# Optimization experiments

Hardware: AMD Instinct MI355X
Metric: run time of the kernel (lower is better)

Reference implementation:

```python
import jax, jax.numpy as jnp
import numpy as np

B, N, M, G = 2, 8192, 8192, 256
X_MIN = Y_MIN = -35.0
CELL = abs(2.0 * X_MIN / G)  # cell size, as in construct_batched_cuda_grid


def setup_inputs() -> dict:
    key = jax.random.key(0)
    k1, k2, k3, k4, k5 = jax.random.split(key, 5)
    p_i = jax.random.uniform(k1, (B, N, 3), jnp.float32, -34.0, 34.0)
    p_j = jax.random.uniform(k2, (B, M, 3), jnp.float32, -34.0, 34.0)
    mos = jax.random.normal(k3, (B, 2, G, G), jnp.float32)
    error_p_i_flow = jax.random.uniform(k4, (B, N), jnp.float32)
    nearest_flow = jax.random.randint(k5, (B, N, 1), 0, M, jnp.int32)
    return {"p_i": p_i, "mos": mos, "p_j": p_j,
            "error_p_i_flow": error_p_i_flow, "nearest_flow": nearest_flow}


def _knn1_l1(x, y):
    # brute-force 1-NN with L1 (norm=1) distance, matching knn_points(..., K=1, norm=1)
    # build (B,N,M) dist one coordinate at a time to avoid a (B,N,M,3) intermediate
    d = (jnp.abs(x[:, :, None, 0] - y[:, None, :, 0])
         + jnp.abs(x[:, :, None, 1] - y[:, None, :, 1])
         + jnp.abs(x[:, :, None, 2] - y[:, None, :, 2]))
    return jnp.min(d, axis=-1), jnp.argmin(d, axis=-1)


def reference(p_i, mos, p_j, error_p_i_flow, nearest_flow):
    # NN_loss with reduction='none' -> error_p_i_rigid = (cham_x + cham_y)/2 (needs N==M)
    cham_x, nearest_rigid = _knn1_l1(p_i, p_j)  # (B,N), (B,N)
    cham_y, _ = _knn1_l1(p_j, p_i)              # (B,M)
    error_p_i_rigid = (cham_x + cham_y) * 0.5

    dynamic = error_p_i_flow > error_p_i_rigid             # (B,N) bool
    idx = jnp.where(dynamic, nearest_flow[..., 0], nearest_rigid)  # (B,N)
    art_labels = dynamic.astype(jnp.int32)                 # (B,N) in {0,1}

    # batched gather p_j[b, idx[b]]
    p_j_by_nn = jnp.take_along_axis(p_j, idx[..., None], axis=1)  # (B,N,3)

    # construct_batched_cuda_grid: scatter labels into (B,G,G), -1 elsewhere
    shift = jnp.array([X_MIN, Y_MIN], jnp.float32)
    cell_idx = ((p_j_by_nn[:, :, :2] - shift) / CELL).astype(jnp.int32)  # (B,N,2)
    bs = jnp.repeat(jnp.arange(B), N)
    grid = -jnp.ones((B, G, G), jnp.int32)
    grid = grid.at[bs,
                   cell_idx[..., 0].reshape(-1),
                   cell_idx[..., 1].reshape(-1)].set(art_labels.reshape(-1))

    # CrossEntropyLoss(ignore_index=-1), mean over non-ignored cells
    logp = jax.nn.log_softmax(mos, axis=1)                 # (B,C,G,G)
    valid = grid >= 0
    tgt = jnp.clip(grid, 0, None)
    lp = jnp.take_along_axis(logp, tgt[:, None], axis=1)[:, 0]  # (B,G,G)
    loss = -jnp.where(valid, lp, 0.0).sum() / jnp.maximum(valid.sum(), 1).astype(lp.dtype)
    return loss
```

## Files before the change

kernel.cpp:

```cpp
#include <hip/hip_runtime.h>
#include <float.h>

#define B_ 2
#define N_ 8192
#define G_ 256
constexpr float X_MIN_F = -35.0f;
constexpr float CELL_F  = 0.2734375f;

using u64 = unsigned long long;

#define OFF_CHAMY 131072
#define OFF_GRID  196608
#define OFF_ACCUM 720896

__global__ __launch_bounds__(256) void init_kernel(uint4* __restrict__ ws)
{
    int i = blockIdx.x * 256 + threadIdx.x;
    if (i < 45056)       ws[i] = make_uint4(~0u, ~0u, ~0u, ~0u);
    else if (i == 45056) ws[i] = make_uint4(0u, 0u, 0u, 0u);
}

template<bool NEED_IDX>
__global__ __launch_bounds__(256) void nn_kernel(const float* __restrict__ P,
                                                 const float* __restrict__ Q,
                                                 u64* __restrict__ outp,
                                                 unsigned* __restrict__ outd)
{
    const int b    = blockIdx.z;
    const int tid  = threadIdx.x;
    const int row0 = blockIdx.x * 1024 + tid * 4;
    const int c0   = blockIdx.y * 128;

    __shared__ __align__(16) float q[128 * 3];
    if (tid < 96)
        ((float4*)q)[tid] = ((const float4*)(Q + ((size_t)b * N_ + c0) * 3))[tid];

    const float4* pp = (const float4*)(P + ((size_t)b * N_ + row0) * 3);
    float4 r0 = pp[0], r1 = pp[1], r2 = pp[2];
    float px[4] = {r0.x, r0.w, r1.z, r2.y};
    float py[4] = {r0.y, r1.x, r1.w, r2.z};
    float pz[4] = {r0.z, r1.y, r2.x, r2.w};

    float best[4]; int bidx[4];
#pragma unroll
    for (int r = 0; r < 4; r++) { best[r] = FLT_MAX; bidx[r] = c0; }

    __syncthreads();

    for (int j4 = 0; j4 < 128; j4 += 4) {
        float4 a  = *(const float4*)&q[j4 * 3];
        float4 bb = *(const float4*)&q[j4 * 3 + 4];
        float4 cc = *(const float4*)&q[j4 * 3 + 8];
        float qxs[4] = {a.x, a.w, bb.z, cc.y};
        float qys[4] = {a.y, bb.x, bb.w, cc.z};
        float qzs[4] = {a.z, bb.y, cc.x, cc.w};
#pragma unroll
        for (int k = 0; k < 4; k++) {
#pragma unroll
            for (int r = 0; r < 4; r++) {
                float d = (fabsf(px[r] - qxs[k]) + fabsf(py[r] - qys[k]))
                          + fabsf(pz[r] - qzs[k]);
                if (NEED_IDX) {
                    bool lt = d < best[r];
                    best[r] = lt ? d : best[r];
                    bidx[r] = lt ? (c0 + j4 + k) : bidx[r];
                } else {
                    best[r] = fminf(best[r], d);
                }
            }
        }
    }

#pragma unroll
    for (int r = 0; r < 4; r++) {
        if (NEED_IDX) {
            u64 pk = ((u64)__float_as_uint(best[r]) << 32) | (unsigned)bidx[r];
            atomicMin(&outp[(size_t)b * N_ + row0 + r], pk);
        } else {
            atomicMin(&outd[(size_t)b * N_ + row0 + r], __float_as_uint(best[r]));
        }
    }
}

__global__ __launch_bounds__(256) void scatter_kernel(
    const u64* __restrict__ chamx, const unsigned* __restrict__ chamy,
    const float* __restrict__ flow, const int* __restrict__ nflow,
    const float* __restrict__ Pj, int* __restrict__ grid)
{
    int i = blockIdx.x * 256 + threadIdx.x;
    int b = i >> 13;
    int n = i & (N_ - 1);

    u64 pX = chamx[i];
    float dx = __uint_as_float((unsigned)(pX >> 32));
    float dy = __uint_as_float(chamy[i]);
    float rigid = (dx + dy) * 0.5f;

    bool dyn  = flow[i] > rigid;
    int label = dyn ? 1 : 0;
    int idx   = dyn ? nflow[i] : (int)(unsigned)(pX & 0xFFFFFFFFull);

    const float* qp = Pj + ((size_t)b * N_ + idx) * 3;
    float x = qp[0], y = qp[1];

    int cx = (int)((x - X_MIN_F) / CELL_F);
    int cy = (int)((y - X_MIN_F) / CELL_F);

    atomicMax(&grid[(b << 16) + cx * G_ + cy], (n << 1) | label);
}

__global__ __launch_bounds__(256) void ce_kernel(const float* __restrict__ mos,
                                                 const int* __restrict__ grid,
                                                 float* __restrict__ accum,
                                                 float* __restrict__ out)
{
    int i = blockIdx.x * 256 + threadIdx.x;
    float lsum = 0.0f;
    int   lcnt = 0;

    int packed = grid[i];
    if (packed >= 0) {
        int b    = i >> 16;
        int cell = i & 0xFFFF;
        float m0 = mos[((size_t)b * 2 + 0) * 65536 + cell];
        float m1 = mos[((size_t)b * 2 + 1) * 65536 + cell];
        float mx = fmaxf(m0, m1);
        float lse = logf(expf(m0 - mx) + expf(m1 - mx));
        float sh  = ((packed & 1) ? m1 : m0) - mx;
        lsum = sh - lse;
        lcnt = 1;
    }

#pragma unroll
    for (int o = 32; o > 0; o >>= 1) {
        lsum += __shfl_down(lsum, o);
        lcnt += __shfl_down(lcnt, o);
    }
    __shared__ float wsum[4];
    __shared__ int   wcnt[4];
    int wave = threadIdx.x >> 6;
    if ((threadIdx.x & 63) == 0) { wsum[wave] = lsum; wcnt[wave] = lcnt; }
    __syncthreads();
    if (threadIdx.x == 0) {
        float s = wsum[0] + wsum[1] + wsum[2] + wsum[3];
        int   c = wcnt[0] + wcnt[1] + wcnt[2] + wcnt[3];
        atomicAdd(&accum[0], s);
        atomicAdd((int*)&accum[1], c);
        __threadfence();
        unsigned t = atomicAdd((unsigned*)&accum[2], 1u);
        if (t == gridDim.x - 1) {
            float S = atomicAdd(&accum[0], 0.0f);
            int   C = atomicAdd((int*)&accum[1], 0);
            out[0] = -S / (float)(C > 0 ? C : 1);
        }
    }
}

extern "C" void kernel_launch(void* const* d_in, const int* in_sizes, int n_in,
                              void* d_out, int out_size, void* d_ws, size_t ws_size,
                              hipStream_t stream)
{
    const float* p_i   = (const float*)d_in[0];
    const float* mos   = (const float*)d_in[1];
    const float* p_j   = (const float*)d_in[2];
    const float* flow  = (const float*)d_in[3];
    const int*   nflow = (const int*)d_in[4];
    float* out = (float*)d_out;

    char* ws = (char*)d_ws;
    u64*      chamx = (u64*)(ws);
    unsigned* chamy = (unsigned*)(ws + OFF_CHAMY);
    int*      grid  = (int*)(ws + OFF_GRID);
    float*    accum = (float*)(ws + OFF_ACCUM);

    init_kernel<<<177, 256, 0, stream>>>((uint4*)ws);

    dim3 g(N_ / 1024, N_ / 128, B_);
    nn_kernel<true ><<<g, 256, 0, stream>>>(p_i, p_j, chamx, nullptr);
    nn_kernel<false><<<g, 256, 0, stream>>>(p_j, p_i, nullptr, chamy);

    scatter_kernel<<<(B_ * N_) / 256, 256, 0, stream>>>(chamx, chamy, flow,
                                                        nflow, p_j, grid);
    ce_kernel<<<(B_ * G_ * G_) / 256, 256, 0, stream>>>(mos, grid, accum, out);
}
```

Baseline: 144.4 us.

## Merge both NN directions into one launch and replace atomics with partial-min buffers

Both nearest-neighbour directions now run in a single kernel launch, with the direction chosen by blockIdx.z. Instead of 64 column chunks doing atomicMin per row, each block handles a larger column chunk (CC of 32 or 4, picked from workspace size) and writes its partial min to its own slot. The scatter kernel then reduces these partials before labelling. This removes one launch and the contention on global atomics, and init now only clears the grid. In exchange it uses more workspace, adds a serial reduction over the partials, and with CC=32 launches fewer blocks (8x32x4), each scanning 256 columns.

After: 148.1 us. 1.03x slower.

```diff
diff --git a/kernel.cpp b/kernel.cpp
--- a/kernel.cpp
+++ b/kernel.cpp
@@ -9,37 +9,42 @@
 
 using u64 = unsigned long long;
 
-#define OFF_CHAMY 131072
-#define OFF_GRID  196608
-#define OFF_ACCUM 720896
-
-__global__ __launch_bounds__(256) void init_kernel(uint4* __restrict__ ws)
+#define OFF_ACCUM 524288
+#define OFF_PX    524544
+
+__global__ __launch_bounds__(256) void init_kernel(uint4* __restrict__ grid4,
+                                                   uint4* __restrict__ accum4)
 {
     int i = blockIdx.x * 256 + threadIdx.x;
-    if (i < 45056)       ws[i] = make_uint4(~0u, ~0u, ~0u, ~0u);
-    else if (i == 45056) ws[i] = make_uint4(0u, 0u, 0u, 0u);
-}
-
-template<bool NEED_IDX>
-__global__ __launch_bounds__(256) void nn_kernel(const float* __restrict__ P,
-                                                 const float* __restrict__ Q,
-                                                 u64* __restrict__ outp,
-                                                 unsigned* __restrict__ outd)
-{
-    const int b    = blockIdx.z;
+    if (i < 32768) grid4[i] = make_uint4(~0u, ~0u, ~0u, ~0u);
+    if (i == 32768) *accum4 = make_uint4(0u, 0u, 0u, 0u);
+}
+
+template<int CC>
+__global__ __launch_bounds__(256) void nn_kernel(const float* __restrict__ p_i,
+                                                 const float* __restrict__ p_j,
+                                                 u64* __restrict__ px,
+                                                 float* __restrict__ py)
+{
+    constexpr int COLS = N_ / CC;
+    const int dir  = blockIdx.z >> 1;
+    const int b    = blockIdx.z & 1;
     const int tid  = threadIdx.x;
     const int row0 = blockIdx.x * 1024 + tid * 4;
-    const int c0   = blockIdx.y * 128;
-
-    __shared__ __align__(16) float q[128 * 3];
-    if (tid < 96)
-        ((float4*)q)[tid] = ((const float4*)(Q + ((size_t)b * N_ + c0) * 3))[tid];
+    const int c0   = blockIdx.y * COLS;
+
+    const float* __restrict__ P = dir ? p_j : p_i;
+    const float* __restrict__ Q = dir ? p_i : p_j;
+
+    __shared__ __align__(16) float q[COLS * 3];
+    for (int t = tid; t < COLS * 3 / 4; t += 256)
+        ((float4*)q)[t] = ((const float4*)(Q + ((size_t)b * N_ + c0) * 3))[t];
 
     const float4* pp = (const float4*)(P + ((size_t)b * N_ + row0) * 3);
     float4 r0 = pp[0], r1 = pp[1], r2 = pp[2];
-    float px[4] = {r0.x, r0.w, r1.z, r2.y};
-    float py[4] = {r0.y, r1.x, r1.w, r2.z};
-    float pz[4] = {r0.z, r1.y, r2.x, r2.w};
+    float px_[4] = {r0.x, r0.w, r1.z, r2.y};
+    float py_[4] = {r0.y, r1.x, r1.w, r2.z};
+    float pz_[4] = {r0.z, r1.y, r2.x, r2.w};
 
     float best[4]; int bidx[4];
 #pragma unroll
@@ -47,43 +52,59 @@
 
     __syncthreads();
 
-    for (int j4 = 0; j4 < 128; j4 += 4) {
-        float4 a  = *(const float4*)&q[j4 * 3];
-        float4 bb = *(const float4*)&q[j4 * 3 + 4];
-        float4 cc = *(const float4*)&q[j4 * 3 + 8];
-        float qxs[4] = {a.x, a.w, bb.z, cc.y};
-        float qys[4] = {a.y, bb.x, bb.w, cc.z};
-        float qzs[4] = {a.z, bb.y, cc.x, cc.w};
-#pragma unroll
-        for (int k = 0; k < 4; k++) {
-#pragma unroll
-            for (int r = 0; r < 4; r++) {
-                float d = (fabsf(px[r] - qxs[k]) + fabsf(py[r] - qys[k]))
-                          + fabsf(pz[r] - qzs[k]);
-                if (NEED_IDX) {
+    if (dir == 0) {
+        for (int j4 = 0; j4 < COLS; j4 += 4) {
+            float4 a  = *(const float4*)&q[j4 * 3];
+            float4 bb = *(const float4*)&q[j4 * 3 + 4];
+            float4 cc = *(const float4*)&q[j4 * 3 + 8];
+            float qx[4] = {a.x, a.w, bb.z, cc.y};
+            float qy[4] = {a.y, bb.x, bb.w, cc.z};
+            float qz[4] = {a.z, bb.y, cc.x, cc.w};
+#pragma unroll
+            for (int k = 0; k < 4; k++) {
+                int jj = c0 + j4 + k;
+#pragma unroll
+                for (int r = 0; r < 4; r++) {
+                    float d = (fabsf(px_[r] - qx[k]) + fabsf(py_[r] - qy[k]))
+                              + fabsf(pz_[r] - qz[k]);
                     bool lt = d < best[r];
                     best[r] = lt ? d : best[r];
-                    bidx[r] = lt ? (c0 + j4 + k) : bidx[r];
-                } else {
+                    bidx[r] = lt ? jj : bidx[r];
+                }
+            }
+        }
+        const size_t o = (size_t)blockIdx.y * (B_ * N_) + b * N_ + row0;
+#pragma unroll
+        for (int r = 0; r < 4; r++) {
+            px[o + r] = ((u64)__float_as_uint(best[r]) << 32) | (unsigned)bidx[r];
+        }
+    } else {
+        for (int j4 = 0; j4 < COLS; j4 += 4) {
+            float4 a  = *(const float4*)&q[j4 * 3];
+            float4 bb = *(const float4*)&q[j4 * 3 + 4];
+            float4 cc = *(const float4*)&q[j4 * 3 + 8];
+            float qx[4] = {a.x, a.w, bb.z, cc.y};
+            float qy[4] = {a.y, bb.x, bb.w, cc.z};
+            float qz[4] = {a.z, bb.y, cc.x, cc.w};
+#pragma unroll
+            for (int k = 0; k < 4; k++) {
+#pragma unroll
+                for (int r = 0; r < 4; r++) {
+                    float d = (fabsf(px_[r] - qx[k]) + fabsf(py_[r] - qy[k]))
+                              + fabsf(pz_[r] - qz[k]);
                     best[r] = fminf(best[r], d);
                 }
             }
         }
-    }
-
-#pragma unroll
-    for (int r = 0; r < 4; r++) {
-        if (NEED_IDX) {
-            u64 pk = ((u64)__float_as_uint(best[r]) << 32) | (unsigned)bidx[r];
-            atomicMin(&outp[(size_t)b * N_ + row0 + r], pk);
-        } else {
-            atomicMin(&outd[(size_t)b * N_ + row0 + r], __float_as_uint(best[r]));
-        }
-    }
-}
-
-__global__ __launch_bounds__(256) void scatter_kernel(
-    const u64* __restrict__ chamx, const unsigned* __restrict__ chamy,
+        const size_t o = (size_t)blockIdx.y * (B_ * N_) + b * N_ + row0;
+#pragma unroll
+        for (int r = 0; r < 4; r++) py[o + r] = best[r];
+    }
+}
+
+template<int CC>
+__global__ __launch_bounds__(256) void reduce_scatter_kernel(
+    const u64* __restrict__ px, const float* __restrict__ py,
     const float* __restrict__ flow, const int* __restrict__ nflow,
     const float* __restrict__ Pj, int* __restrict__ grid)
 {
@@ -91,14 +112,22 @@
     int b = i >> 13;
     int n = i & (N_ - 1);
 
-    u64 pX = chamx[i];
-    float dx = __uint_as_float((unsigned)(pX >> 32));
-    float dy = __uint_as_float(chamy[i]);
-    float rigid = (dx + dy) * 0.5f;
+    u64 bx = px[i];
+#pragma unroll 4
+    for (int c = 1; c < CC; c++) {
+        u64 v = px[(size_t)c * (B_ * N_) + i];
+        bx = v < bx ? v : bx;
+    }
+    float by = py[i];
+#pragma unroll 4
+    for (int c = 1; c < CC; c++) by = fminf(by, py[(size_t)c * (B_ * N_) + i]);
+
+    float dx = __uint_as_float((unsigned)(bx >> 32));
+    float rigid = (dx + by) * 0.5f;
 
     bool dyn  = flow[i] > rigid;
     int label = dyn ? 1 : 0;
-    int idx   = dyn ? nflow[i] : (int)(unsigned)(pX & 0xFFFFFFFFull);
+    int idx   = dyn ? nflow[i] : (int)(unsigned)(bx & 0xFFFFFFFFull);
 
     const float* qp = Pj + ((size_t)b * N_ + idx) * 3;
     float x = qp[0], y = qp[1];
@@ -156,6 +185,26 @@
     }
 }
 
+template<int CC>
+static void run(const float* p_i, const float* mos, const float* p_j,
+                const float* flow, const int* nflow, float* out,
+                char* ws, hipStream_t stream)
+{
+    int*   grid  = (int*)ws;
+    float* accum = (float*)(ws + OFF_ACCUM);
+    u64*   px    = (u64*)(ws + OFF_PX);
+    float* py    = (float*)(ws + OFF_PX + (size_t)CC * B_ * N_ * 8);
+
+    init_kernel<<<129, 256, 0, stream>>>((uint4*)grid, (uint4*)accum);
+
+    dim3 g(N_ / 1024, CC, 4);
+    nn_kernel<CC><<<g, 256, 0, stream>>>(p_i, p_j, px, py);
+
+    reduce_scatter_kernel<CC><<<(B_ * N_) / 256, 256, 0, stream>>>(
+        px, py, flow, nflow, p_j, grid);
+    ce_kernel<<<(B_ * G_ * G_) / 256, 256, 0, stream>>>(mos, grid, accum, out);
+}
+
 extern "C" void kernel_launch(void* const* d_in, const int* in_sizes, int n_in,
                               void* d_out, int out_size, void* d_ws, size_t ws_size,
                               hipStream_t stream)
@@ -166,20 +215,10 @@
     const float* flow  = (const float*)d_in[3];
     const int*   nflow = (const int*)d_in[4];
     float* out = (float*)d_out;
-
     char* ws = (char*)d_ws;
-    u64*      chamx = (u64*)(ws);
-    unsigned* chamy = (unsigned*)(ws + OFF_CHAMY);
-    int*      grid  = (int*)(ws + OFF_GRID);
-    float*    accum = (float*)(ws + OFF_ACCUM);
-
-    init_kernel<<<177, 256, 0, stream>>>((uint4*)ws);
-
-    dim3 g(N_ / 1024, N_ / 128, B_);
-    nn_kernel<true ><<<g, 256, 0, stream>>>(p_i, p_j, chamx, nullptr);
-    nn_kernel<false><<<g, 256, 0, stream>>>(p_j, p_i, nullptr, chamy);
-
-    scatter_kernel<<<(B_ * N_) / 256, 256, 0, stream>>>(chamx, chamy, flow,
-                                                        nflow, p_j, grid);
-    ce_kernel<<<(B_ * G_ * G_) / 256, 256, 0, stream>>>(mos, grid, accum, out);
-}
+
+    if (ws_size >= OFF_PX + (size_t)32 * B_ * N_ * 12)
+        run<32>(p_i, mos, p_j, flow, nflow, out, ws, stream);
+    else
+        run<4>(p_i, mos, p_j, flow, nflow, out, ws, stream);
+}
```

## Replace brute-force L1 nearest-neighbour with uniform-grid spatial search

Applied to the files above, without the earlier changes.

Bins both point sets into a 16^3 uniform grid (with fixed per-cell capacity and an overflow list), then searches the 27 neighbouring cells with four threads per query, followed by ring expansion until the L1 bound guarantees exactness. Both chamfer directions are computed in one kernel, and grid/accumulator initialisation is folded into the binning kernel. This removes the O(N*M) all-pairs distance work. In exchange it adds atomics for binning, divergent per-query loops, and correctness that depends on the ring-termination bound and the overflow handling. Tie-breaking now compares packed original indices, which preserves lowest-index selection.

Measured after the change: 185.4 us. +28.4%, slower.

```diff
diff --git a/kernel.cpp b/kernel.cpp
--- a/kernel.cpp
+++ b/kernel.cpp
@@ -7,78 +7,154 @@
 constexpr float X_MIN_F = -35.0f;
 constexpr float CELL_F  = 0.2734375f;
 
+#define GC   16
+#define GS   4.375f
+#define CAP  32
+
 using u64 = unsigned long long;
 
-#define OFF_CHAMY 131072
-#define OFF_GRID  196608
-#define OFF_ACCUM 720896
-
-__global__ __launch_bounds__(256) void init_kernel(uint4* __restrict__ ws)
-{
-    int i = blockIdx.x * 256 + threadIdx.x;
-    if (i < 45056)       ws[i] = make_uint4(~0u, ~0u, ~0u, ~0u);
-    else if (i == 45056) ws[i] = make_uint4(0u, 0u, 0u, 0u);
-}
-
-template<bool NEED_IDX>
-__global__ __launch_bounds__(256) void nn_kernel(const float* __restrict__ P,
-                                                 const float* __restrict__ Q,
-                                                 u64* __restrict__ outp,
-                                                 unsigned* __restrict__ outd)
-{
-    const int b    = blockIdx.z;
+#define OFF_ACCUM 524288
+#define OFF_CHAMX 524352
+#define OFF_CHAMY 655424
+#define OFF_CNT   720960
+#define OFF_OCNT  786496
+#define OFF_CELLS 786560
+#define OFF_OFLOW 9175168
+
+__device__ __forceinline__ int cell_of(float x) {
+    int c = (int)((x + 35.0f) * (1.0f / GS));
+    return c < 0 ? 0 : (c > 15 ? 15 : c);
+}
+
+__global__ __launch_bounds__(256) void bin_kernel(
+    const float* __restrict__ p_i, const float* __restrict__ p_j,
+    int* __restrict__ cnt, int* __restrict__ ocnt,
+    float4* __restrict__ cells, float4* __restrict__ oflow,
+    int* __restrict__ grid, unsigned* __restrict__ accum)
+{
+    const int pi = blockIdx.x * 256 + threadIdx.x;
+
+    ((uint4*)grid)[pi] = make_uint4(~0u, ~0u, ~0u, ~0u);
+    if (pi < 4) accum[pi] = 0u;
+
+    const int set = pi >> 14;
+    const int b   = (pi >> 13) & 1;
+    const int n   = pi & (N_ - 1);
+    const float* src = set ? p_i : p_j;
+    const float* pp  = src + ((size_t)b * N_ + n) * 3;
+    float x = pp[0], y = pp[1], z = pp[2];
+    const int g = b * 2 + set;
+    const int cell = (cell_of(x) << 8) | (cell_of(y) << 4) | cell_of(z);
+
+    float4 rec = make_float4(x, y, z, __uint_as_float((unsigned)n));
+    int slot = atomicAdd(&cnt[(g << 12) | cell], 1);
+    if (slot < CAP)
+        cells[(((size_t)(g << 12) | cell) << 5) + slot] = rec;
+    else {
+        int o = atomicAdd(&ocnt[g], 1);
+        oflow[((size_t)g << 13) + o] = rec;
+    }
+}
+
+__global__ __launch_bounds__(256) void nn_grid_kernel(
+    const float* __restrict__ p_i, const float* __restrict__ p_j,
+    const int* __restrict__ cnt, const int* __restrict__ ocnt,
+    const float4* __restrict__ cells, const float4* __restrict__ oflow,
+    u64* __restrict__ chamx, unsigned* __restrict__ chamy)
+{
+    __shared__ u64 sb[64];
     const int tid  = threadIdx.x;
-    const int row0 = blockIdx.x * 1024 + tid * 4;
-    const int c0   = blockIdx.y * 128;
-
-    __shared__ __align__(16) float q[128 * 3];
-    if (tid < 96)
-        ((float4*)q)[tid] = ((const float4*)(Q + ((size_t)b * N_ + c0) * 3))[tid];
-
-    const float4* pp = (const float4*)(P + ((size_t)b * N_ + row0) * 3);
-    float4 r0 = pp[0], r1 = pp[1], r2 = pp[2];
-    float px[4] = {r0.x, r0.w, r1.z, r2.y};
-    float py[4] = {r0.y, r1.x, r1.w, r2.z};
-    float pz[4] = {r0.z, r1.y, r2.x, r2.w};
-
-    float best[4]; int bidx[4];
-#pragma unroll
-    for (int r = 0; r < 4; r++) { best[r] = FLT_MAX; bidx[r] = c0; }
-
+    const int ql   = tid >> 2;
+    const int role = tid & 3;
+    const int qg   = blockIdx.x * 64 + ql;
+    const int dir  = qg >> 14;
+    const int b    = (qg >> 13) & 1;
+    const int n    = qg & (N_ - 1);
+
+    const float* Qp = dir ? p_j : p_i;
+    const float* qp = Qp + ((size_t)b * N_ + n) * 3;
+    const float qx = qp[0], qy = qp[1], qz = qp[2];
+    const int g  = b * 2 + dir;
+    const int cx = cell_of(qx), cy = cell_of(qy), cz = cell_of(qz);
+
+    if (tid < 64) sb[tid] = ~0ull;
     __syncthreads();
 
-    for (int j4 = 0; j4 < 128; j4 += 4) {
-        float4 a  = *(const float4*)&q[j4 * 3];
-        float4 bb = *(const float4*)&q[j4 * 3 + 4];
-        float4 cc = *(const float4*)&q[j4 * 3 + 8];
-        float qxs[4] = {a.x, a.w, bb.z, cc.y};
-        float qys[4] = {a.y, bb.x, bb.w, cc.z};
-        float qzs[4] = {a.z, bb.y, cc.x, cc.w};
-#pragma unroll
-        for (int k = 0; k < 4; k++) {
-#pragma unroll
-            for (int r = 0; r < 4; r++) {
-                float d = (fabsf(px[r] - qxs[k]) + fabsf(py[r] - qys[k]))
-                          + fabsf(pz[r] - qzs[k]);
-                if (NEED_IDX) {
-                    bool lt = d < best[r];
-                    best[r] = lt ? d : best[r];
-                    bidx[r] = lt ? (c0 + j4 + k) : bidx[r];
-                } else {
-                    best[r] = fminf(best[r], d);
+    u64 best = ~0ull;
+    {
+        int l = 0;
+        for (int dx = -1; dx <= 1; dx++)
+            for (int dy = -1; dy <= 1; dy++)
+                for (int dz = -1; dz <= 1; dz++, l++) {
+                    if ((l & 3) != role) continue;
+                    int ax = cx + dx, ay = cy + dy, az = cz + dz;
+                    if ((unsigned)ax > 15u || (unsigned)ay > 15u ||
+                        (unsigned)az > 15u) continue;
+                    int cell = (ax << 8) | (ay << 4) | az;
+                    int c = cnt[(g << 12) | cell];
+                    c = c > CAP ? CAP : c;
+                    const float4* base =
+                        cells + (((size_t)(g << 12) | cell) << 5);
+                    for (int k = 0; k < c; k++) {
+                        float4 pt = base[k];
+                        float d = (fabsf(qx - pt.x) + fabsf(qy - pt.y))
+                                  + fabsf(qz - pt.z);
+                        u64 pk = ((u64)__float_as_uint(d) << 32)
+                                 | (unsigned)__float_as_uint(pt.w);
+                        best = pk < best ? pk : best;
+                    }
                 }
-            }
+    }
+    atomicMin(&sb[ql], best);
+    __syncthreads();
+
+    if (role == 0) {
+        best = sb[ql];
+
+        for (int r = 2; r <= 15; r++) {
+            unsigned db = (unsigned)(best >> 32);
+            float bd = (db == 0xFFFFFFFFu) ? FLT_MAX : __uint_as_float(db);
+            if ((float)(r - 1) * 4.3f > bd) break;
+            for (int dx = -r; dx <= r; dx++)
+                for (int dy = -r; dy <= r; dy++)
+                    for (int dz = -r; dz <= r; dz++) {
+                        int mx = dx < 0 ? -dx : dx;
+                        int my = dy < 0 ? -dy : dy;
+                        int mz = dz < 0 ? -dz : dz;
+                        int m = mx > my ? mx : my;
+                        m = m > mz ? m : mz;
+                        if (m != r) continue;
+                        int ax = cx + dx, ay = cy + dy, az = cz + dz;
+                        if ((unsigned)ax > 15u || (unsigned)ay > 15u ||
+                            (unsigned)az > 15u) continue;
+                        int cell = (ax << 8) | (ay << 4) | az;
+                        int c = cnt[(g << 12) | cell];
+                        c = c > CAP ? CAP : c;
+                        const float4* base =
+                            cells + (((size_t)(g << 12) | cell) << 5);
+                        for (int k = 0; k < c; k++) {
+                            float4 pt = base[k];
+                            float d = (fabsf(qx - pt.x) + fabsf(qy - pt.y))
+                                      + fabsf(qz - pt.z);
+                            u64 pk = ((u64)__float_as_uint(d) << 32)
+                                     | (unsigned)__float_as_uint(pt.w);
+                            best = pk < best ? pk : best;
+                        }
+                    }
         }
-    }
-
-#pragma unroll
-    for (int r = 0; r < 4; r++) {
-        if (NEED_IDX) {
-            u64 pk = ((u64)__float_as_uint(best[r]) << 32) | (unsigned)bidx[r];
-            atomicMin(&outp[(size_t)b * N_ + row0 + r], pk);
-        } else {
-            atomicMin(&outd[(size_t)b * N_ + row0 + r], __float_as_uint(best[r]));
+
+        int oc = ocnt[g];
+        for (int k = 0; k < oc; k++) {
+            float4 pt = oflow[((size_t)g << 13) + k];
+            float d = (fabsf(qx - pt.x) + fabsf(qy - pt.y))
+                      + fabsf(qz - pt.z);
+            u64 pk = ((u64)__float_as_uint(d) << 32)
+                     | (unsigned)__float_as_uint(pt.w);
+            best = pk < best ? pk : best;
         }
+
+        if (dir == 0) chamx[(size_t)b * N_ + n] = best;
+        else          chamy[(size_t)b * N_ + n] = (unsigned)(best >> 32);
     }
 }
 
@@ -166,19 +242,23 @@
     const float* flow  = (const float*)d_in[3];
     const int*   nflow = (const int*)d_in[4];
     float* out = (float*)d_out;
-
     char* ws = (char*)d_ws;
-    u64*      chamx = (u64*)(ws);
+
+    int*      grid  = (int*)ws;
+    float*    accum = (float*)(ws + OFF_ACCUM);
+    u64*      chamx = (u64*)(ws + OFF_CHAMX);
     unsigned* chamy = (unsigned*)(ws + OFF_CHAMY);
-    int*      grid  = (int*)(ws + OFF_GRID);
-    float*    accum = (float*)(ws + OFF_ACCUM);
-
-    init_kernel<<<177, 256, 0, stream>>>((uint4*)ws);
-
-    dim3 g(N_ / 1024, N_ / 128, B_);
-    nn_kernel<true ><<<g, 256, 0, stream>>>(p_i, p_j, chamx, nullptr);
-    nn_kernel<false><<<g, 256, 0, stream>>>(p_j, p_i, nullptr, chamy);
-
+    int*      cnt   = (int*)(ws + OFF_CNT);
+    int*      ocnt  = (int*)(ws + OFF_OCNT);
+    float4*   cells = (float4*)(ws + OFF_CELLS);
+    float4*   oflow = (float4*)(ws + OFF_OFLOW);
+
+    hipMemsetAsync(ws + OFF_CNT, 0, OFF_CELLS - OFF_CNT, stream);
+
+    bin_kernel<<<128, 256, 0, stream>>>(p_i, p_j, cnt, ocnt, cells, oflow,
+                                        grid, (unsigned*)accum);
+    nn_grid_kernel<<<512, 256, 0, stream>>>(p_i, p_j, cnt, ocnt, cells, oflow,
+                                            chamx, chamy);
     scatter_kernel<<<(B_ * N_) / 256, 256, 0, stream>>>(chamx, chamy, flow,
                                                         nflow, p_j, grid);
     ce_kernel<<<(B_ * G_ * G_) / 256, 256, 0, stream>>>(mos, grid, accum, out);
```
